# Kernel tuning notes

Measured on AMD Instinct MI355X. Metric: run time of the kernel, lower is better.

The kernel has to match this reference:

```python
import jax, jax.numpy as jnp
import numpy as np

B, HOR, E, L = 16, 512, 1024, 12
ACT_NUM, DIM, ADIM = 10, 64, 10
N = 2 * HOR                      # backbone sequence length (test=False)
NPOS = 4 * (1 + HOR)             # wpe table size
D_IN = 3 + DIM * ACT_NUM + ADIM  # embed_transition input dim = 653


def setup_inputs() -> dict:
    key = jax.random.key(0)
    ks = jax.random.split(key, 12)
    s = lambda k, shape: (jax.random.normal(k, shape, jnp.float32) * 0.02)
    return {
        "action_set": jax.random.normal(ks[0], (B, ACT_NUM, DIM), jnp.float32),
        "context_rewards": jax.random.normal(ks[1], (B, HOR, 1), jnp.float32),
        "wpe": s(ks[2], (NPOS, E)),
        "W_emb": s(ks[3], (D_IN, E)),
        "b_emb": jnp.zeros((E,), jnp.float32),
        "Wq": s(ks[4], (L, E, E)),
        "Wk": s(ks[5], (L, E, E)),
        "Wv": s(ks[6], (L, E, E)),
        "ln1_g": jnp.ones((L, E), jnp.float32),
        "ln1_b": jnp.zeros((L, E), jnp.float32),
        "W1": s(ks[7], (L, E, E)),
        "b1": jnp.zeros((L, E), jnp.float32),
        "W2": s(ks[8], (L, E, E)),
        "b2": jnp.zeros((L, E), jnp.float32),
        "ln2_g": jnp.ones((L, E), jnp.float32),
        "ln2_b": jnp.zeros((L, E), jnp.float32),
        "W_pred": s(ks[9], (E, ADIM)),
        "b_pred": jnp.zeros((ADIM,), jnp.float32),
    }


def _layernorm(x, g, b, eps=1e-5):
    mu = x.mean(-1, keepdims=True)
    var = ((x - mu) ** 2).mean(-1, keepdims=True)
    return (x - mu) * jax.lax.rsqrt(var + eps) * g + b


def reference(action_set, context_rewards, wpe, W_emb, b_emb, Wq, Wk, Wv,
              ln1_g, ln1_b, W1, b1, W2, b2, ln2_g, ln2_b, W_pred, b_pred):
    batch = action_set.shape[0]
    hor = context_rewards.shape[1]
    n = 2 * hor
    # --- build interleaved sequence (outer Transformer glue) ---
    a = action_set.reshape(batch, 1, -1)                       # [B,1,DA]
    pair = jnp.concatenate([a, jnp.zeros_like(a)], axis=1)     # [B,2,DA]
    act_set_seq = jnp.tile(pair, (1, hor, 1))                  # [B,2H,DA]
    action_seq = jnp.zeros((batch, n, ADIM + 1), jnp.float32)
    one_seq = jnp.ones((batch, n, 1), jnp.float32)
    pos_seq = jnp.broadcast_to(
        jnp.arange(1, n + 1, dtype=jnp.float32).reshape(1, n, 1), (batch, n, 1))
    seq = jnp.concatenate([act_set_seq, action_seq, one_seq, pos_seq], axis=2)  # [B,N,D_IN]
    # --- DecoderTransformerBackbone ---
    Hs = seq @ W_emb + b_emb
    Hs = Hs + wpe[:n]                                          # positional embedding
    idx = jnp.arange(n)
    # normalized causal mask: row i has 1/(i+1) on j<=i, else 0
    mask = jnp.where(idx[:, None] >= idx[None, :],
                     1.0 / (idx[:, None].astype(jnp.float32) + 1.0), 0.0)
    for l in range(Wq.shape[0]):
        q = Hs @ Wq[l]
        k = Hs @ Wk[l]
        v = Hs @ Wv[l]
        attn = jax.nn.relu(jnp.einsum('bid,bjd->bij', q, k)) * mask
        Hs = Hs + jnp.einsum('bij,bjd->bid', attn, v)
        Hs = _layernorm(Hs, ln1_g[l], ln1_b[l])
        Hs = Hs + (jax.nn.relu(Hs @ W1[l] + b1[l]) @ W2[l] + b2[l])
        Hs = _layernorm(Hs, ln2_g[l], ln2_b[l])
    preds = Hs @ W_pred + b_pred                               # [B,N,ADIM]
    return preds[:, 0::2, :]                                   # [B,HOR,ADIM]
```

## Files before the change

### kernel.cpp

```cpp
#include <hip/hip_runtime.h>
#include <stdint.h>
#include <stddef.h>

#define E_DIM 1024
#define B_SZ  16
#define N_SEQ 1024
#define L_NUM 12
#define ACT_D 640
#define ADIM_ 10

typedef unsigned short u16;
typedef __attribute__((ext_vector_type(8))) short bf16x8;
typedef __attribute__((ext_vector_type(4))) float f32x4;

__device__ __forceinline__ u16 f2bf(float x) {
  union { float f; unsigned int u; } c; c.f = x;
  unsigned int r = c.u + 0x7fffu + ((c.u >> 16) & 1u);
  return (u16)(r >> 16);
}
__device__ __forceinline__ float bf2f(u16 h) {
  union { unsigned int u; float f; } c; c.u = ((unsigned int)h) << 16;
  return c.f;
}

struct us4 { u16 x, y, z, w; };

#define GLD16(gsrc, ldst) __builtin_amdgcn_global_load_lds( \
    (const __attribute__((address_space(1))) void*)(gsrc),  \
    (__attribute__((address_space(3))) void*)(ldst), 16, 0, 0)

#define TM 128
#define TN 128
#define TK 32

template<int MODE, int EPI>
__global__ __launch_bounds__(256)
void gemm_nt_mfma(const u16* __restrict__ Ah, const u16* __restrict__ Al,
                  const u16* __restrict__ Bh0, const u16* __restrict__ Bl0,
                  const u16* __restrict__ Bh1, const u16* __restrict__ Bl1,
                  float* __restrict__ Co,
                  u16* __restrict__ Ch0, u16* __restrict__ Cl0,
                  u16* __restrict__ Ch1, u16* __restrict__ Cl1,
                  const float* __restrict__ bias0, const float* __restrict__ bias1,
                  int K, int lda, int ldb, int ldc, int tilesN,
                  long long sA, long long sB, long long sC)
{
  __shared__ u16 smem[2 * 4 * TM * TK];

  const int tid = threadIdx.x;
  const int bat = blockIdx.y;

  const u16* Bh = Bh0; const u16* Bl = Bl0;
  u16* Ch = Ch0; u16* Cl = Cl0;
  const float* bias = bias0;
  if (blockIdx.z) { Bh = Bh1; Bl = Bl1; Ch = Ch1; Cl = Cl1; bias = bias1; }

  Ah += bat * sA; Al += bat * sA;
  Bh += bat * sB; Bl += bat * sB;

  int bid;
  {
    const int nwg = gridDim.x;
    const int q = nwg >> 3, r = nwg & 7;
    const int xcd = blockIdx.x & 7, off = blockIdx.x >> 3;
    bid = ((xcd < r) ? xcd * (q + 1) : r * (q + 1) + (xcd - r) * q) + off;
  }

  int tm, tn;
  if (MODE == 1) {
    int t = bid, m = 0;
    while ((m + 1) * (m + 2) / 2 <= t) m++;
    tm = m; tn = t - m * (m + 1) / 2;
  } else {
    tm = bid / tilesN;
    tn = bid % tilesN;
  }
  int kend = K;
  if (MODE == 2) { int c = (tm + 1) * TM; kend = (c < K) ? c : K; }
  const int nk = kend / TK;

  const int c0 = tid, c1 = tid + 256;
  const int r0 = c0 >> 2, r1 = c1 >> 2;
  const int p0 = ((c0 & 3) ^ ((r0 >> 1) & 3)) * 8;
  const int p1 = ((c1 & 3) ^ ((r1 >> 1) & 3)) * 8;
  const u16* gAh0 = Ah + (long long)(tm * TM + r0) * lda + p0;
  const u16* gAh1 = Ah + (long long)(tm * TM + r1) * lda + p1;
  const u16* gAl0 = Al + (long long)(tm * TM + r0) * lda + p0;
  const u16* gAl1 = Al + (long long)(tm * TM + r1) * lda + p1;
  const u16* gBh0 = Bh + (long long)(tn * TN + r0) * ldb + p0;
  const u16* gBh1 = Bh + (long long)(tn * TN + r1) * ldb + p1;
  const u16* gBl0 = Bl + (long long)(tn * TN + r0) * ldb + p0;
  const u16* gBl1 = Bl + (long long)(tn * TN + r1) * ldb + p1;
  const int o0 = c0 * 8, o1 = c1 * 8;

  auto stage = [&](int buf) {
    u16* base = smem + buf * 16384;
    GLD16(gAh0, base + o0);          GLD16(gAh1, base + o1);
    GLD16(gAl0, base + 4096 + o0);   GLD16(gAl1, base + 4096 + o1);
    GLD16(gBh0, base + 8192 + o0);   GLD16(gBh1, base + 8192 + o1);
    GLD16(gBl0, base + 12288 + o0);  GLD16(gBl1, base + 12288 + o1);
    gAh0 += TK; gAh1 += TK; gAl0 += TK; gAl1 += TK;
    gBh0 += TK; gBh1 += TK; gBl0 += TK; gBl1 += TK;
  };

  const int lane = tid & 63;
  const int w = tid >> 6, wr = w >> 1, wc = w & 1;
  const int fr = lane & 15;
  const int kq = (lane >> 4) * 8;
  const int sa = ((fr >> 1) & 3) << 3;
  const int aoff = ((wr * 64 + fr) * TK + kq) ^ sa;
  const int boff = ((wc * 64 + fr) * TK + kq) ^ sa;

  f32x4 acc[4][4];
  #pragma unroll
  for (int m = 0; m < 4; m++)
    #pragma unroll
    for (int n = 0; n < 4; n++) acc[m][n] = (f32x4){0.f, 0.f, 0.f, 0.f};

  stage(0);
  __syncthreads();

  for (int t = 0; t < nk; t++) {
    if (t + 1 < nk) stage((t + 1) & 1);
    const u16* sb = smem + (t & 1) * 16384;

    bf16x8 ah[4], al[4], bh[4], bl[4];
    #pragma unroll
    for (int m = 0; m < 4; m++) ah[m] = *(const bf16x8*)(sb + aoff + m * 512);
    #pragma unroll
    for (int n = 0; n < 4; n++) bh[n] = *(const bf16x8*)(sb + 8192 + boff + n * 512);
    #pragma unroll
    for (int m = 0; m < 4; m++)
      #pragma unroll
      for (int n = 0; n < 4; n++)
        acc[m][n] = __builtin_amdgcn_mfma_f32_16x16x32_bf16(ah[m], bh[n], acc[m][n], 0, 0, 0);
    #pragma unroll
    for (int n = 0; n < 4; n++) bl[n] = *(const bf16x8*)(sb + 12288 + boff + n * 512);
    #pragma unroll
    for (int m = 0; m < 4; m++)
      #pragma unroll
      for (int n = 0; n < 4; n++)
        acc[m][n] = __builtin_amdgcn_mfma_f32_16x16x32_bf16(ah[m], bl[n], acc[m][n], 0, 0, 0);
    #pragma unroll
    for (int m = 0; m < 4; m++) al[m] = *(const bf16x8*)(sb + 4096 + aoff + m * 512);
    #pragma unroll
    for (int m = 0; m < 4; m++)
      #pragma unroll
      for (int n = 0; n < 4; n++)
        acc[m][n] = __builtin_amdgcn_mfma_f32_16x16x32_bf16(al[m], bh[n], acc[m][n], 0, 0, 0);

    __syncthreads();
  }

  if (Co) Co += bat * sC;
  if (Ch) { Ch += bat * sC; Cl += bat * sC; }
  #pragma unroll
  for (int m = 0; m < 4; m++) {
    #pragma unroll
    for (int r = 0; r < 4; r++) {
      const long long row = (long long)tm * TM + wr * 64 + m * 16 + (lane >> 4) * 4 + r;
      #pragma unroll
      for (int n = 0; n < 4; n++) {
        const long long col = (long long)tn * TN + wc * 64 + n * 16 + (lane & 15);
        float v = acc[m][n][r];
        if (EPI == 2) { v += bias[col]; v = v > 0.f ? v : 0.f; }
        if (EPI == 4) { v += bias[col]; }
        if (EPI == 3) {
          v = v > 0.f ? v : 0.f;
          v = (col <= row) ? v / (float)(row + 1) : 0.f;
        }
        const long long idx = row * (long long)ldc + col;
        if (EPI == 0 || EPI == 4) {
          Co[idx] = v;
        } else {
          u16 h = f2bf(v);
          Ch[idx] = h;
          Cl[idx] = f2bf(v - bf2f(h));
        }
      }
    }
  }
}

struct TP3 {
  const float* s0; const float* s1; const float* s2;
  u16* h0; u16* l0; u16* h1; u16* l1; u16* h2; u16* l2;
};

__global__ __launch_bounds__(256)
void transpose_split3(TP3 p)
{
  __shared__ float tile[32][33];
  const float* src; u16* dh; u16* dl;
  if (blockIdx.z == 0)      { src = p.s0; dh = p.h0; dl = p.l0; }
  else if (blockIdx.z == 1) { src = p.s1; dh = p.h1; dl = p.l1; }
  else                      { src = p.s2; dh = p.h2; dl = p.l2; }
  const int c0 = blockIdx.x * 32, r0 = blockIdx.y * 32;
  const int tx = threadIdx.x & 31, ty = threadIdx.x >> 5;
  #pragma unroll
  for (int i = ty; i < 32; i += 8)
    tile[i][tx] = src[(long long)(r0 + i) * E_DIM + c0 + tx];
  __syncthreads();
  #pragma unroll
  for (int i = ty; i < 32; i += 8) {
    const float v = tile[tx][i];
    const u16 h = f2bf(v);
    const long long idx = (long long)(c0 + i) * E_DIM + r0 + tx;
    dh[idx] = h;
    dl[idx] = f2bf(v - bf2f(h));
  }
}

__global__ __launch_bounds__(256)
void resid_ln(u16* __restrict__ hh, u16* __restrict__ hl,
              const float* __restrict__ delta,
              const float* __restrict__ g, const float* __restrict__ bta)
{
  __shared__ float red[8];
  const long long row = blockIdx.x;
  u16* hp = hh + row * E_DIM;
  u16* lp = hl + row * E_DIM;
  const float* dp = delta + row * E_DIM;
  const int tid = threadIdx.x;
  const int e = tid * 4;

  us4 hv = *(const us4*)(hp + e);
  us4 lv = *(const us4*)(lp + e);
  float4 d = *(const float4*)(dp + e);
  float x0 = bf2f(hv.x) + bf2f(lv.x) + d.x;
  float x1 = bf2f(hv.y) + bf2f(lv.y) + d.y;
  float x2 = bf2f(hv.z) + bf2f(lv.z) + d.z;
  float x3 = bf2f(hv.w) + bf2f(lv.w) + d.w;
  float s = x0 + x1 + x2 + x3;
  float q = x0 * x0 + x1 * x1 + x2 * x2 + x3 * x3;
  #pragma unroll
  for (int o = 32; o > 0; o >>= 1) { s += __shfl_down(s, o); q += __shfl_down(q, o); }
  const int lane = tid & 63, wv = tid >> 6;
  if (lane == 0) { red[wv] = s; red[wv + 4] = q; }
  __syncthreads();
  const float st = red[0] + red[1] + red[2] + red[3];
  const float qt = red[4] + red[5] + red[6] + red[7];
  const float mu = st * (1.0f / E_DIM);
  const float var = qt * (1.0f / E_DIM) - mu * mu;
  const float rstd = rsqrtf(var + 1e-5f);

  float4 gg = *(const float4*)(g + e);
  float4 bb = *(const float4*)(bta + e);
  float y0 = (x0 - mu) * rstd * gg.x + bb.x;
  float y1 = (x1 - mu) * rstd * gg.y + bb.y;
  float y2 = (x2 - mu) * rstd * gg.z + bb.z;
  float y3 = (x3 - mu) * rstd * gg.w + bb.w;

  us4 ho, lo;
  ho.x = f2bf(y0); lo.x = f2bf(y0 - bf2f(ho.x));
  ho.y = f2bf(y1); lo.y = f2bf(y1 - bf2f(ho.y));
  ho.z = f2bf(y2); lo.z = f2bf(y2 - bf2f(ho.z));
  ho.w = f2bf(y3); lo.w = f2bf(y3 - bf2f(ho.w));
  *(us4*)(hp + e) = ho;
  *(us4*)(lp + e) = lo;
}

__global__ __launch_bounds__(256)
void emb_dot(const float* __restrict__ act, const float* __restrict__ Wemb,
             float* __restrict__ Aemb)
{
  const int e = blockIdx.x * 256 + threadIdx.x;
  const int b = blockIdx.y;
  const float* ab = act + b * ACT_D;
  float s = 0.f;
  for (int d = 0; d < ACT_D; d++)
    s = fmaf(ab[d], Wemb[(long long)d * E_DIM + e], s);
  Aemb[b * E_DIM + e] = s;
}

__global__ __launch_bounds__(256)
void emb_fill(const float* __restrict__ Aemb, const float* __restrict__ Wemb,
              const float* __restrict__ bemb, const float* __restrict__ wpe,
              u16* __restrict__ oh, u16* __restrict__ ol)
{
  const int i = blockIdx.x, b = blockIdx.y;
  const int e = threadIdx.x * 4;
  float4 a;
  if ((i & 1) == 0) a = *(const float4*)(Aemb + b * E_DIM + e);
  else { a.x = 0.f; a.y = 0.f; a.z = 0.f; a.w = 0.f; }
  float4 be = *(const float4*)(bemb + e);
  float4 w1 = *(const float4*)(Wemb + 651LL * E_DIM + e);
  float4 w2 = *(const float4*)(Wemb + 652LL * E_DIM + e);
  float4 pw = *(const float4*)(wpe + (long long)i * E_DIM + e);
  const float pos = (float)(i + 1);
  float y0 = a.x + be.x + w1.x + pos * w2.x + pw.x;
  float y1 = a.y + be.y + w1.y + pos * w2.y + pw.y;
  float y2 = a.z + be.z + w1.z + pos * w2.z + pw.z;
  float y3 = a.w + be.w + w1.w + pos * w2.w + pw.w;
  const long long row = (long long)b * N_SEQ + i;

  us4 ho, lo;
  ho.x = f2bf(y0); lo.x = f2bf(y0 - bf2f(ho.x));
  ho.y = f2bf(y1); lo.y = f2bf(y1 - bf2f(ho.y));
  ho.z = f2bf(y2); lo.z = f2bf(y2 - bf2f(ho.z));
  ho.w = f2bf(y3); lo.w = f2bf(y3 - bf2f(ho.w));
  *(us4*)(oh + row * E_DIM + e) = ho;
  *(us4*)(ol + row * E_DIM + e) = lo;
}

__global__ __launch_bounds__(256)
void pred_k(const u16* __restrict__ hh, const u16* __restrict__ hl,
            const float* __restrict__ Wp, const float* __restrict__ bp,
            float* __restrict__ out)
{
  __shared__ float part[4][ADIM_];
  const int h = blockIdx.x, b = blockIdx.y;
  const long long row = (long long)b * N_SEQ + 2 * h;
  const u16* xh = hh + row * E_DIM;
  const u16* xl = hl + row * E_DIM;
  float acc[ADIM_];
  #pragma unroll
  for (int a = 0; a < ADIM_; a++) acc[a] = 0.f;
  for (int e = threadIdx.x; e < E_DIM; e += 256) {
    const float xv = bf2f(xh[e]) + bf2f(xl[e]);
    const float* wq = Wp + e * ADIM_;
    #pragma unroll
    for (int a = 0; a < ADIM_; a++) acc[a] = fmaf(xv, wq[a], acc[a]);
  }
  const int lane = threadIdx.x & 63, wv = threadIdx.x >> 6;
  #pragma unroll
  for (int a = 0; a < ADIM_; a++)
    #pragma unroll
    for (int o = 32; o > 0; o >>= 1) acc[a] += __shfl_down(acc[a], o);
  if (lane == 0)
    #pragma unroll
    for (int a = 0; a < ADIM_; a++) part[wv][a] = acc[a];
  __syncthreads();
  if (threadIdx.x < ADIM_) {
    const int a = threadIdx.x;
    out[((long long)b * (N_SEQ / 2) + h) * ADIM_ + a] =
        part[0][a] + part[1][a] + part[2][a] + part[3][a] + bp[a];
  }
}

__global__ __launch_bounds__(256)
void fill_sentinel(float* p, int n, float v)
{
  int i = blockIdx.x * 256 + threadIdx.x;
  if (i < n) p[i] = v;
}

extern "C" void kernel_launch(void* const* d_in, const int* in_sizes, int n_in,
                              void* d_out, int out_size, void* d_ws, size_t ws_size,
                              hipStream_t stream)
{
  const float* act  = (const float*)d_in[0];
  const float* wpe  = (const float*)d_in[2];
  const float* Wemb = (const float*)d_in[3];
  const float* bemb = (const float*)d_in[4];
  const float* Wq   = (const float*)d_in[5];
  const float* Wk   = (const float*)d_in[6];
  const float* Wv   = (const float*)d_in[7];
  const float* ln1g = (const float*)d_in[8];
  const float* ln1b = (const float*)d_in[9];
  const float* W1   = (const float*)d_in[10];
  const float* b1   = (const float*)d_in[11];
  const float* W2   = (const float*)d_in[12];
  const float* b2   = (const float*)d_in[13];
  const float* ln2g = (const float*)d_in[14];
  const float* ln2b = (const float*)d_in[15];
  const float* Wp   = (const float*)d_in[16];
  const float* bp   = (const float*)d_in[17];
  float* out = (float*)d_out;

  const long long sQ = (long long)N_SEQ * E_DIM;
  const long long sE = (long long)E_DIM * E_DIM;

  auto need = [&](int G) -> size_t {
    return (size_t)G * sQ * 16 + (size_t)sE * 12
         + (size_t)G * E_DIM * 4 + (size_t)(1 << 20);
  };
  int G = 16;
  while (G > 1 && need(G) > ws_size) G >>= 1;
  if (need(G) > ws_size || d_ws == nullptr) {
    fill_sentinel<<<dim3((out_size + 255) / 256), 256, 0, stream>>>(out, out_size, 1.0e7f);
    return;
  }

  char* ws = (char*)d_ws;
  size_t off = 0;
  auto alloc = [&](size_t bytes) -> void* {
    void* p = ws + off;
    off += (bytes + 255) & ~(size_t)255;
    return p;
  };
  u16* hsh = (u16*)alloc((size_t)G * sQ * 2);
  u16* hsl = (u16*)alloc((size_t)G * sQ * 2);
  u16* qh  = (u16*)alloc((size_t)G * sQ * 2);
  u16* ql  = (u16*)alloc((size_t)G * sQ * 2);
  char* kreg = (char*)alloc((size_t)G * sQ * 4);
  u16* kh = (u16*)kreg;
  u16* kl = kh + (size_t)G * sQ;
  float* dbuf = (float*)kreg;
  u16* sh_ = (u16*)alloc((size_t)G * sQ * 2);
  u16* sl_ = (u16*)alloc((size_t)G * sQ * 2);
  u16* wAh = (u16*)alloc((size_t)sE * 2);
  u16* wAl = (u16*)alloc((size_t)sE * 2);
  u16* wBh = (u16*)alloc((size_t)sE * 2);
  u16* wBl = (u16*)alloc((size_t)sE * 2);
  u16* wCh = (u16*)alloc((size_t)sE * 2);
  u16* wCl = (u16*)alloc((size_t)sE * 2);
  float* Aemb = (float*)alloc((size_t)G * E_DIM * 4);

  const int tE = E_DIM / TN;
  const int tS = N_SEQ / TN;
  const int triS = tS * (tS + 1) / 2;
  const dim3 gqk((G * N_SEQ / TM) * tE, 1, 2);
  const dim3 gm ((G * N_SEQ / TM) * tE, 1, 1);
  const dim3 gsq(triS, G, 1);
  const dim3 gv (tE * tS, G, 1);

  for (int g0 = 0; g0 < B_SZ; g0 += G) {
    emb_dot<<<dim3(E_DIM / 256, G), 256, 0, stream>>>(act + (long long)g0 * ACT_D, Wemb, Aemb);
    emb_fill<<<dim3(N_SEQ, G), 256, 0, stream>>>(Aemb, Wemb, bemb, wpe, hsh, hsl);

    for (int l = 0; l < L_NUM; l++) {
      const long long wof = (long long)l * sE;
      const long long bof = (long long)l * E_DIM;

      TP3 t2 = {Wq + wof, Wk + wof, Wq + wof, wAh, wAl, wBh, wBl, wAh, wAl};
      transpose_split3<<<dim3(32, 32, 2), 256, 0, stream>>>(t2);
      gemm_nt_mfma<0, 1><<<gqk, 256, 0, stream>>>(hsh, hsl, wAh, wAl, wBh, wBl,
          nullptr, qh, ql, kh, kl, nullptr, nullptr,
          E_DIM, E_DIM, E_DIM, E_DIM, tE, 0, 0, 0);

      TP3 t3 = {Wv + wof, W1 + wof, W2 + wof, wAh, wAl, wBh, wBl, wCh, wCl};
      transpose_split3<<<dim3(32, 32, 3), 256, 0, stream>>>(t3);

      gemm_nt_mfma<1, 3><<<gsq, 256, 0, stream>>>(qh, ql, kh, kl, kh, kl,
          nullptr, sh_, sl_, sh_, sl_, nullptr, nullptr,
          E_DIM, E_DIM, E_DIM, N_SEQ, tS, sQ, sQ, sQ);

      gemm_nt_mfma<0, 1><<<gv, 256, 0, stream>>>(wAh, wAl, hsh, hsl, hsh, hsl,
          nullptr, qh, ql, qh, ql, nullptr, nullptr,
          E_DIM, E_DIM, E_DIM, N_SEQ, tS, 0, sQ, sQ);

      gemm_nt_mfma<2, 0><<<gv, 256, 0, stream>>>(sh_, sl_, qh, ql, qh, ql,
          dbuf, nullptr, nullptr, nullptr, nullptr, nullptr, nullptr,
          N_SEQ, N_SEQ, N_SEQ, E_DIM, tE, sQ, sQ, sQ);

      resid_ln<<<dim3(G * N_SEQ), 256, 0, stream>>>(hsh, hsl, dbuf,
          ln1g + bof, ln1b + bof);

      gemm_nt_mfma<0, 2><<<gm, 256, 0, stream>>>(hsh, hsl, wBh, wBl, wBh, wBl,
          nullptr, qh, ql, qh, ql, b1 + bof, b1 + bof,
          E_DIM, E_DIM, E_DIM, E_DIM, tE, 0, 0, 0);
      gemm_nt_mfma<0, 4><<<gm, 256, 0, stream>>>(qh, ql, wCh, wCl, wCh, wCl,
          dbuf, nullptr, nullptr, nullptr, nullptr, b2 + bof, b2 + bof,
          E_DIM, E_DIM, E_DIM, E_DIM, tE, 0, 0, 0);

      resid_ln<<<dim3(G * N_SEQ), 256, 0, stream>>>(hsh, hsl, dbuf,
          ln2g + bof, ln2b + bof);
    }

    pred_k<<<dim3(N_SEQ / 2, G), 256, 0, stream>>>(hsh, hsl, Wp, bp,
        out + (long long)g0 * (N_SEQ / 2) * ADIM_);
  }
}
```

Baseline: 9.510 ms.

## Enlarge GEMM tile to 256x128 with 512 threads and triple-buffered LDS pipeline

```diff
diff --git a/kernel.cpp b/kernel.cpp
--- a/kernel.cpp
+++ b/kernel.cpp
@@ -29,12 +29,15 @@
     (const __attribute__((address_space(1))) void*)(gsrc),  \
     (__attribute__((address_space(3))) void*)(ldst), 16, 0, 0)
 
-#define TM 128
-#define TN 128
-#define TK 32
+#define BM 256
+#define BN 128
+#define BK 32
+#define LDS_A 8192
+#define LDS_B 4096
+#define BUFU 24576
 
 template<int MODE, int EPI>
-__global__ __launch_bounds__(256)
+__global__ __launch_bounds__(512)
 void gemm_nt_mfma(const u16* __restrict__ Ah, const u16* __restrict__ Al,
                   const u16* __restrict__ Bh0, const u16* __restrict__ Bl0,
                   const u16* __restrict__ Bh1, const u16* __restrict__ Bl1,
@@ -45,7 +48,7 @@
                   int K, int lda, int ldb, int ldc, int tilesN,
                   long long sA, long long sB, long long sC)
 {
-  __shared__ u16 smem[2 * 4 * TM * TK];
+  __shared__ u16 smem[3 * BUFU];
 
   const int tid = threadIdx.x;
   const int bat = blockIdx.y;
@@ -69,99 +72,113 @@
   int tm, tn;
   if (MODE == 1) {
     int t = bid, m = 0;
-    while ((m + 1) * (m + 2) / 2 <= t) m++;
-    tm = m; tn = t - m * (m + 1) / 2;
+    while ((m + 1) * (m + 2) <= t) m++;
+    tm = m; tn = t - m * (m + 1);
   } else {
     tm = bid / tilesN;
     tn = bid % tilesN;
   }
   int kend = K;
-  if (MODE == 2) { int c = (tm + 1) * TM; kend = (c < K) ? c : K; }
-  const int nk = kend / TK;
-
-  const int c0 = tid, c1 = tid + 256;
-  const int r0 = c0 >> 2, r1 = c1 >> 2;
-  const int p0 = ((c0 & 3) ^ ((r0 >> 1) & 3)) * 8;
-  const int p1 = ((c1 & 3) ^ ((r1 >> 1) & 3)) * 8;
-  const u16* gAh0 = Ah + (long long)(tm * TM + r0) * lda + p0;
-  const u16* gAh1 = Ah + (long long)(tm * TM + r1) * lda + p1;
-  const u16* gAl0 = Al + (long long)(tm * TM + r0) * lda + p0;
-  const u16* gAl1 = Al + (long long)(tm * TM + r1) * lda + p1;
-  const u16* gBh0 = Bh + (long long)(tn * TN + r0) * ldb + p0;
-  const u16* gBh1 = Bh + (long long)(tn * TN + r1) * ldb + p1;
-  const u16* gBl0 = Bl + (long long)(tn * TN + r0) * ldb + p0;
-  const u16* gBl1 = Bl + (long long)(tn * TN + r1) * ldb + p1;
-  const int o0 = c0 * 8, o1 = c1 * 8;
-
-  auto stage = [&](int buf) {
-    u16* base = smem + buf * 16384;
-    GLD16(gAh0, base + o0);          GLD16(gAh1, base + o1);
-    GLD16(gAl0, base + 4096 + o0);   GLD16(gAl1, base + 4096 + o1);
-    GLD16(gBh0, base + 8192 + o0);   GLD16(gBh1, base + 8192 + o1);
-    GLD16(gBl0, base + 12288 + o0);  GLD16(gBl1, base + 12288 + o1);
-    gAh0 += TK; gAh1 += TK; gAl0 += TK; gAl1 += TK;
-    gBh0 += TK; gBh1 += TK; gBl0 += TK; gBl1 += TK;
+  if (MODE == 2) { int c = (tm + 1) * BM; kend = (c < K) ? c : K; }
+  const int nk = kend / BK;
+
+  const int ca0 = tid, ca1 = tid + 512, cb0 = tid;
+  const int ra0 = ca0 >> 2, ra1 = ca1 >> 2, rb0 = cb0 >> 2;
+  const int pa0 = ((ca0 & 3) ^ ((ra0 >> 1) & 3)) * 8;
+  const int pa1 = ((ca1 & 3) ^ ((ra1 >> 1) & 3)) * 8;
+  const int pb0 = ((cb0 & 3) ^ ((rb0 >> 1) & 3)) * 8;
+  const u16* gAh0 = Ah + (long long)(tm * BM + ra0) * lda + pa0;
+  const u16* gAh1 = Ah + (long long)(tm * BM + ra1) * lda + pa1;
+  const u16* gAl0 = Al + (long long)(tm * BM + ra0) * lda + pa0;
+  const u16* gAl1 = Al + (long long)(tm * BM + ra1) * lda + pa1;
+  const u16* gBh0 = Bh + (long long)(tn * BN + rb0) * ldb + pb0;
+  const u16* gBl0 = Bl + (long long)(tn * BN + rb0) * ldb + pb0;
+  const int oa0 = ca0 * 8, oa1 = ca1 * 8, ob0 = cb0 * 8;
+
+  int issued = 0;
+  auto stage = [&]() {
+    u16* base = smem + (issued % 3) * BUFU;
+    GLD16(gAh0, base + oa0);
+    GLD16(gAh1, base + oa1);
+    GLD16(gAl0, base + LDS_A + oa0);
+    GLD16(gAl1, base + LDS_A + oa1);
+    GLD16(gBh0, base + 2 * LDS_A + ob0);
+    GLD16(gBl0, base + 2 * LDS_A + LDS_B + ob0);
+    gAh0 += BK; gAh1 += BK; gAl0 += BK; gAl1 += BK;
+    gBh0 += BK; gBl0 += BK;
+    issued++;
   };
 
   const int lane = tid & 63;
-  const int w = tid >> 6, wr = w >> 1, wc = w & 1;
+  const int w = tid >> 6, wr = w >> 2, wc = w & 3;
   const int fr = lane & 15;
   const int kq = (lane >> 4) * 8;
   const int sa = ((fr >> 1) & 3) << 3;
-  const int aoff = ((wr * 64 + fr) * TK + kq) ^ sa;
-  const int boff = ((wc * 64 + fr) * TK + kq) ^ sa;
-
-  f32x4 acc[4][4];
-  #pragma unroll
-  for (int m = 0; m < 4; m++)
-    #pragma unroll
-    for (int n = 0; n < 4; n++) acc[m][n] = (f32x4){0.f, 0.f, 0.f, 0.f};
-
-  stage(0);
-  __syncthreads();
+  const int aoff = ((wr * 128 + fr) * BK + kq) ^ sa;
+  const int boff = ((wc * 32 + fr) * BK + kq) ^ sa;
+
+  f32x4 acc[8][2];
+  #pragma unroll
+  for (int m = 0; m < 8; m++)
+    #pragma unroll
+    for (int n = 0; n < 2; n++) acc[m][n] = (f32x4){0.f, 0.f, 0.f, 0.f};
+
+  stage(); stage();
+  asm volatile("s_waitcnt vmcnt(6)" ::: "memory");
+  __builtin_amdgcn_s_barrier();
 
   for (int t = 0; t < nk; t++) {
-    if (t + 1 < nk) stage((t + 1) & 1);
-    const u16* sb = smem + (t & 1) * 16384;
-
-    bf16x8 ah[4], al[4], bh[4], bl[4];
-    #pragma unroll
-    for (int m = 0; m < 4; m++) ah[m] = *(const bf16x8*)(sb + aoff + m * 512);
-    #pragma unroll
-    for (int n = 0; n < 4; n++) bh[n] = *(const bf16x8*)(sb + 8192 + boff + n * 512);
-    #pragma unroll
-    for (int m = 0; m < 4; m++)
+    if (issued < nk) stage();
+    const u16* sb = smem + (t % 3) * BUFU;
+
+    bf16x8 ah[8], al[8], bh[2], bl[2];
+    #pragma unroll
+    for (int m = 0; m < 8; m++) ah[m] = *(const bf16x8*)(sb + aoff + m * (16 * BK));
+    #pragma unroll
+    for (int n = 0; n < 2; n++) bh[n] = *(const bf16x8*)(sb + 2 * LDS_A + boff + n * (16 * BK));
+    __builtin_amdgcn_s_setprio(1);
+    #pragma unroll
+    for (int m = 0; m < 8; m++)
       #pragma unroll
-      for (int n = 0; n < 4; n++)
+      for (int n = 0; n < 2; n++)
         acc[m][n] = __builtin_amdgcn_mfma_f32_16x16x32_bf16(ah[m], bh[n], acc[m][n], 0, 0, 0);
-    #pragma unroll
-    for (int n = 0; n < 4; n++) bl[n] = *(const bf16x8*)(sb + 12288 + boff + n * 512);
-    #pragma unroll
-    for (int m = 0; m < 4; m++)
+    __builtin_amdgcn_s_setprio(0);
+    #pragma unroll
+    for (int n = 0; n < 2; n++) bl[n] = *(const bf16x8*)(sb + 2 * LDS_A + LDS_B + boff + n * (16 * BK));
+    __builtin_amdgcn_s_setprio(1);
+    #pragma unroll
+    for (int m = 0; m < 8; m++)
       #pragma unroll
-      for (int n = 0; n < 4; n++)
+      for (int n = 0; n < 2; n++)
         acc[m][n] = __builtin_amdgcn_mfma_f32_16x16x32_bf16(ah[m], bl[n], acc[m][n], 0, 0, 0);
-    #pragma unroll
-    for (int m = 0; m < 4; m++) al[m] = *(const bf16x8*)(sb + 4096 + aoff + m * 512);
-    #pragma unroll
-    for (int m = 0; m < 4; m++)
+    __builtin_amdgcn_s_setprio(0);
+    #pragma unroll
+    for (int m = 0; m < 8; m++) al[m] = *(const bf16x8*)(sb + LDS_A + aoff + m * (16 * BK));
+    __builtin_amdgcn_s_setprio(1);
+    #pragma unroll
+    for (int m = 0; m < 8; m++)
       #pragma unroll
-      for (int n = 0; n < 4; n++)
+      for (int n = 0; n < 2; n++)
         acc[m][n] = __builtin_amdgcn_mfma_f32_16x16x32_bf16(al[m], bh[n], acc[m][n], 0, 0, 0);
-
-    __syncthreads();
+    __builtin_amdgcn_s_setprio(0);
+
+    if (t + 1 < nk) {
+      if (issued > t + 2) asm volatile("s_waitcnt vmcnt(6)" ::: "memory");
+      else                asm volatile("s_waitcnt vmcnt(0)" ::: "memory");
+      __builtin_amdgcn_s_barrier();
+    }
   }
 
   if (Co) Co += bat * sC;
   if (Ch) { Ch += bat * sC; Cl += bat * sC; }
   #pragma unroll
-  for (int m = 0; m < 4; m++) {
+  for (int m = 0; m < 8; m++) {
     #pragma unroll
     for (int r = 0; r < 4; r++) {
-      const long long row = (long long)tm * TM + wr * 64 + m * 16 + (lane >> 4) * 4 + r;
+      const long long row = (long long)tm * BM + wr * 128 + m * 16 + (lane >> 4) * 4 + r;
       #pragma unroll
-      for (int n = 0; n < 4; n++) {
-        const long long col = (long long)tn * TN + wc * 64 + n * 16 + (lane & 15);
+      for (int n = 0; n < 2; n++) {
+        const long long col = (long long)tn * BN + wc * 32 + n * 16 + (lane & 15);
         float v = acc[m][n][r];
         if (EPI == 2) { v += bias[col]; v = v > 0.f ? v : 0.f; }
         if (EPI == 4) { v += bias[col]; }
@@ -377,7 +394,7 @@
   };
   int G = 16;
   while (G > 1 && need(G) > ws_size) G >>= 1;
-  if (need(G) > ws_size || d_ws == nullptr) {
+  if (need(G) > ws_size || d_ws == nullptr || G < 8) {
     fill_sentinel<<<dim3((out_size + 255) / 256), 256, 0, stream>>>(out, out_size, 1.0e7f);
     return;
   }
@@ -407,13 +424,12 @@
   u16* wCl = (u16*)alloc((size_t)sE * 2);
   float* Aemb = (float*)alloc((size_t)G * E_DIM * 4);
 
-  const int tE = E_DIM / TN;
-  const int tS = N_SEQ / TN;
-  const int triS = tS * (tS + 1) / 2;
-  const dim3 gqk((G * N_SEQ / TM) * tE, 1, 2);
-  const dim3 gm ((G * N_SEQ / TM) * tE, 1, 1);
+  const int tE = E_DIM / BN;
+  const int triS = 20;
+  const dim3 gqk((G * N_SEQ / BM) * tE, 1, 2);
+  const dim3 gm ((G * N_SEQ / BM) * tE, 1, 1);
   const dim3 gsq(triS, G, 1);
-  const dim3 gv (tE * tS, G, 1);
+  const dim3 gv ((N_SEQ / BM) * tE, G, 1);
 
   for (int g0 = 0; g0 < B_SZ; g0 += G) {
     emb_dot<<<dim3(E_DIM / 256, G), 256, 0, stream>>>(act + (long long)g0 * ACT_D, Wemb, Aemb);
@@ -425,32 +441,32 @@
 
       TP3 t2 = {Wq + wof, Wk + wof, Wq + wof, wAh, wAl, wBh, wBl, wAh, wAl};
       transpose_split3<<<dim3(32, 32, 2), 256, 0, stream>>>(t2);
-      gemm_nt_mfma<0, 1><<<gqk, 256, 0, stream>>>(hsh, hsl, wAh, wAl, wBh, wBl,
+      gemm_nt_mfma<0, 1><<<gqk, 512, 0, stream>>>(hsh, hsl, wAh, wAl, wBh, wBl,
           nullptr, qh, ql, kh, kl, nullptr, nullptr,
           E_DIM, E_DIM, E_DIM, E_DIM, tE, 0, 0, 0);
 
       TP3 t3 = {Wv + wof, W1 + wof, W2 + wof, wAh, wAl, wBh, wBl, wCh, wCl};
       transpose_split3<<<dim3(32, 32, 3), 256, 0, stream>>>(t3);
 
-      gemm_nt_mfma<1, 3><<<gsq, 256, 0, stream>>>(qh, ql, kh, kl, kh, kl,
+      gemm_nt_mfma<1, 3><<<gsq, 512, 0, stream>>>(qh, ql, kh, kl, kh, kl,
           nullptr, sh_, sl_, sh_, sl_, nullptr, nullptr,
-          E_DIM, E_DIM, E_DIM, N_SEQ, tS, sQ, sQ, sQ);
-
-      gemm_nt_mfma<0, 1><<<gv, 256, 0, stream>>>(wAh, wAl, hsh, hsl, hsh, hsl,
+          E_DIM, E_DIM, E_DIM, N_SEQ, tE, sQ, sQ, sQ);
+
+      gemm_nt_mfma<0, 1><<<gv, 512, 0, stream>>>(wAh, wAl, hsh, hsl, hsh, hsl,
           nullptr, qh, ql, qh, ql, nullptr, nullptr,
-          E_DIM, E_DIM, E_DIM, N_SEQ, tS, 0, sQ, sQ);
-
-      gemm_nt_mfma<2, 0><<<gv, 256, 0, stream>>>(sh_, sl_, qh, ql, qh, ql,
+          E_DIM, E_DIM, E_DIM, N_SEQ, tE, 0, sQ, sQ);
+
+      gemm_nt_mfma<2, 0><<<gv, 512, 0, stream>>>(sh_, sl_, qh, ql, qh, ql,
           dbuf, nullptr, nullptr, nullptr, nullptr, nullptr, nullptr,
           N_SEQ, N_SEQ, N_SEQ, E_DIM, tE, sQ, sQ, sQ);
 
       resid_ln<<<dim3(G * N_SEQ), 256, 0, stream>>>(hsh, hsl, dbuf,
           ln1g + bof, ln1b + bof);
 
-      gemm_nt_mfma<0, 2><<<gm, 256, 0, stream>>>(hsh, hsl, wBh, wBl, wBh, wBl,
+      gemm_nt_mfma<0, 2><<<gm, 512, 0, stream>>>(hsh, hsl, wBh, wBl, wBh, wBl,
           nullptr, qh, ql, qh, ql, b1 + bof, b1 + bof,
           E_DIM, E_DIM, E_DIM, E_DIM, tE, 0, 0, 0);
-      gemm_nt_mfma<0, 4><<<gm, 256, 0, stream>>>(qh, ql, wCh, wCl, wCh, wCl,
+      gemm_nt_mfma<0, 4><<<gm, 512, 0, stream>>>(qh, ql, wCh, wCl, wCh, wCl,
           dbuf, nullptr, nullptr, nullptr, nullptr, b2 + bof, b2 + bof,
           E_DIM, E_DIM, E_DIM, E_DIM, tE, 0, 0, 0);
 
```

After: 9.224 ms. 1.03x faster.
